# Kernel tuning notes

Hardware: AMD Instinct MI355X
Metric: run time of the kernel (lower is better)

Reference implementation:

```python
import jax, jax.numpy as jnp
import numpy as np

D_MODEL = 1024
RANK = 256
INIT_ALPHA = 0.5


def setup_inputs() -> dict:
    key = jax.random.key(0)
    ks = jax.random.split(key, 12)
    D, R = D_MODEL, RANK
    s = 0.02
    return {
        "x": jax.random.normal(ks[0], (4, 2048, D), dtype=jnp.float32),
        "Wq": jax.random.normal(ks[1], (D, D), dtype=jnp.float32) * s,
        "Wk": jax.random.normal(ks[2], (D, D), dtype=jnp.float32) * s,
        "Wo": jax.random.normal(ks[3], (D, D), dtype=jnp.float32) * s,
        "U_b": jax.random.normal(ks[4], (D, R), dtype=jnp.float32) * s,
        "V_b": jax.random.normal(ks[5], (D, R), dtype=jnp.float32) * s,
        "W_b": jax.random.normal(ks[6], (D, R), dtype=jnp.float32) * s,
        "bias_b": jnp.zeros((D,), dtype=jnp.float32),
        "U_t": jax.random.normal(ks[7], (D, R), dtype=jnp.float32) * s,
        "V_t": jax.random.normal(ks[8], (D, R), dtype=jnp.float32) * s,
        "W_t": jax.random.normal(ks[9], (D, R), dtype=jnp.float32) * s,
        "X_t": jax.random.normal(ks[10], (D, R), dtype=jnp.float32) * s,
        "bias_t": jnp.zeros((D,), dtype=jnp.float32),
        "alpha": jnp.asarray(INIT_ALPHA, dtype=jnp.float32),
    }


def reference(x, Wq, Wk, Wo, U_b, V_b, W_b, bias_b, U_t, V_t, W_t, X_t, bias_t, alpha):
    # Math identical to the original O(T^2 D) materialization (attention_mask=None path),
    # reduced to causal cumulative sums: sum_{j<=i} (q_i * k_j) = q_i * cumsum_j(k_j).
    B, T, D = x.shape
    Q = x @ Wq.T                      # [B,T,D] (nn.Linear: x @ W^T)
    K = x @ Wk.T
    counts = jnp.arange(1, T + 1, dtype=x.dtype)[None, :, None]  # [1,T,1]
    Z = jnp.cumsum(x, axis=1) / counts  # causal cumulative mean [B,T,D]

    # Bilinear: sum_{j<=i} ((Q_i V_b) * (K_j W_b)) U_b^T + bias_b (per j)
    a_b = Q @ V_b                     # [B,T,R]
    c_b = jnp.cumsum(K @ W_b, axis=1) # [B,T,R] causal sum over j
    bil = (a_b * c_b) @ U_b.T         # [B,T,D]

    # Trilinear: sum_{j<=i} ((Q_i V_t) * (K_j W_t) * (Z_i X_t)) U_t^T + bias_t
    a_t = Q @ V_t
    c_t = jnp.cumsum(K @ W_t, axis=1)
    z_t = Z @ X_t
    tri = (a_t * z_t * c_t) @ U_t.T   # [B,T,D]

    # Per-i division by n_valid = i+1; the per-(i,j) biases average back to themselves.
    out = (bil + alpha * tri) / counts + (bias_b + alpha * bias_t)
    return out @ Wo.T                 # W_O (dropout=0 -> identity)
```

## Files before the change

kernel.cpp:

```cpp
#include <hip/hip_runtime.h>

#define NBATCH  4
#define TSEQ    2048
#define MROWS   8192
#define NCAT    1280
#define NE      512

#define OFF_WQT   0u
#define OFF_WKT   524288u
#define OFF_WOB   1048576u
#define OFF_VCT   1572864u
#define OFF_WCT   1835008u
#define OFF_UCT   2097152u
#define OFF_B2    2359296u
#define OFF_PB    2360320u
#define OFF_GB    3015680u
#define OFF_Y     3277824u
#define OFF_SCR   13763584u
#define OFF_XB    13861888u
#define OFF_EB    OFF_XB

typedef __attribute__((ext_vector_type(8))) short bf16x8;
typedef __attribute__((ext_vector_type(4))) float f32x4;

__device__ __forceinline__ unsigned short f2bf(float f) {
  union { float f; unsigned u; } v; v.f = f;
  return (unsigned short)((v.u + 0x7fff + ((v.u >> 16) & 1)) >> 16);
}

__device__ __forceinline__ void gload16(const void* g, void* l) {
  __builtin_amdgcn_global_load_lds(
      (const __attribute__((address_space(1))) unsigned*)g,
      (__attribute__((address_space(3))) unsigned*)l, 16, 0, 0);
}

template <int EPI, int OBF, int CS>
__device__ __forceinline__ void mfma_tile(
    const short* __restrict__ A, const short* __restrict__ B, void* __restrict__ Cv,
    int K, int ldA, int ldB, int ldC, int m0, int n0,
    const float* __restrict__ bias, float* __restrict__ scr, short* L) {
  short* As = L;
  short* Bs = L + 8192;
  const int tid = threadIdx.x;
  const int l = tid & 63;
  const int wv = tid >> 6;
  const int wm = (wv >> 1) * 64, wn = (wv & 1) * 64;
  const int srow = tid >> 3;
  const int schk = tid & 7;
  const int arow = wm + (l & 15), brow = wn + (l & 15);
  const int kq = l >> 4;

  f32x4 acc[4][4] = {};

  for (int k0 = 0; k0 < K; k0 += 64) {
#pragma unroll
    for (int p = 0; p < 4; ++p) {
      const int r = p * 32 + srow;
      const int sw = (schk ^ (r & 7)) * 8;
      gload16(A + (size_t)(m0 + r) * ldA + k0 + sw, As + r * 64 + schk * 8);
      gload16(B + (size_t)(n0 + r) * ldB + k0 + sw, Bs + r * 64 + schk * 8);
    }
    __syncthreads();
#pragma unroll
    for (int h = 0; h < 2; ++h) {
      bf16x8 af[4], bfr[4];
#pragma unroll
      for (int m = 0; m < 4; ++m) {
        const int r = arow + m * 16;
        af[m] = *(const bf16x8*)&As[r * 64 + (((h * 4 + kq) ^ (r & 7)) * 8)];
      }
#pragma unroll
      for (int n = 0; n < 4; ++n) {
        const int r = brow + n * 16;
        bfr[n] = *(const bf16x8*)&Bs[r * 64 + (((h * 4 + kq) ^ (r & 7)) * 8)];
      }
#pragma unroll
      for (int m = 0; m < 4; ++m)
#pragma unroll
        for (int n = 0; n < 4; ++n)
          acc[m][n] = __builtin_amdgcn_mfma_f32_16x16x32_bf16(af[m], bfr[n], acc[m][n], 0, 0, 0);
    }
    __syncthreads();
  }

  const int cc = wn + (l & 15);
  const int crb = wm + (l >> 4) * 4;
#pragma unroll
  for (int m = 0; m < 4; ++m) {
#pragma unroll
    for (int j = 0; j < 4; ++j) {
      const int gm = m0 + crb + m * 16 + j;
      float inv = 1.0f;
      if (EPI) inv = 1.0f / (float)((gm & (TSEQ - 1)) + 1);
#pragma unroll
      for (int n = 0; n < 4; ++n) {
        const int gn = n0 + cc + n * 16;
        float v = acc[m][n][j];
        if (EPI) v = v * inv + bias[gn];
        if (OBF) ((short*)Cv)[(size_t)gm * ldC + gn] = (short)f2bf(v);
        else     ((float*)Cv)[(size_t)gm * ldC + gn] = v;
      }
    }
  }
  if (CS && n0 >= 512) {
    const int bb = (m0 + wm) >> 11;
    const int seg = ((m0 + wm) & (TSEQ - 1)) >> 6;
    float* sp = scr + (size_t)(bb * 32 + seg) * 768 + (n0 - 512);
#pragma unroll
    for (int n = 0; n < 4; ++n) {
      float s = 0.f;
#pragma unroll
      for (int m = 0; m < 4; ++m)
#pragma unroll
        for (int j = 0; j < 4; ++j) s += acc[m][n][j];
      s += __shfl_xor(s, 16, 64);
      s += __shfl_xor(s, 32, 64);
      if (l < 16) sp[cc + n * 16] = s;
    }
  }
}

template <int EPI, int CS>
__global__ __launch_bounds__(256) void mfma_nt(
    const short* __restrict__ A, const short* __restrict__ B,
    float* __restrict__ C, int K, int ldA, int ldB, int ldC,
    const float* __restrict__ bias, float* __restrict__ scr) {
  __shared__ short L[16384];
  mfma_tile<EPI, 0, CS>(A, B, C, K, ldA, ldB, ldC,
                        blockIdx.y * 128, blockIdx.x * 128, bias, scr, L);
}

__global__ __launch_bounds__(256) void prep_mfma(
    const short* __restrict__ VCT, const short* __restrict__ WQT,
    const short* __restrict__ WCT, const short* __restrict__ WKT,
    const short* __restrict__ WOB, const short* __restrict__ UCT,
    short* __restrict__ Pb, short* __restrict__ Gb) {
  __shared__ short L[16384];
  const int g = blockIdx.x >> 5, t = blockIdx.x & 31;
  if (g == 0)
    mfma_tile<0, 1, 0>(VCT, WQT, Pb, 1024, 1024, 1024, 1024,
                       (t >> 3) * 128, (t & 7) * 128, nullptr, nullptr, L);
  else if (g == 1)
    mfma_tile<0, 1, 0>(WCT, WKT, Pb + (size_t)512 * 1024, 1024, 1024, 1024, 1024,
                       (t >> 3) * 128, (t & 7) * 128, nullptr, nullptr, L);
  else
    mfma_tile<0, 1, 0>(WOB, UCT, Gb, 1024, 1024, 1024, 512,
                       (t >> 2) * 128, (t & 3) * 128, nullptr, nullptr, L);
}

__global__ __launch_bounds__(256) void prep_all(
    const float* __restrict__ Vb, const float* __restrict__ Vt,
    const float* __restrict__ Wb, const float* __restrict__ Wt,
    const float* __restrict__ Ub, const float* __restrict__ Ut,
    const float* __restrict__ Xt, const float* __restrict__ Wq,
    const float* __restrict__ Wk, const float* __restrict__ Wo,
    const float* __restrict__ x,
    const float* __restrict__ bias_b, const float* __restrict__ bias_t,
    const float* __restrict__ alpha_p,
    short* __restrict__ VCT, short* __restrict__ WCT, short* __restrict__ UCT,
    short* __restrict__ PbXt, short* __restrict__ WQT, short* __restrict__ WKT,
    short* __restrict__ WOB, short* __restrict__ xb, float* __restrict__ b2) {
  const int bid = blockIdx.x;
  const int tid = threadIdx.x;
  if (bid >= 10176) {
    const float al = *alpha_p;
    const int d = bid - 10176;
    float s = 0.f;
    for (int e = tid; e < 1024; e += 256)
      s += Wo[(size_t)d * 1024 + e] * (bias_b[e] + al * bias_t[e]);
    __shared__ float red[256];
    red[tid] = s; __syncthreads();
    for (int off = 128; off > 0; off >>= 1) {
      if (tid < off) red[tid] += red[tid + off];
      __syncthreads();
    }
    if (tid == 0) b2[d] = red[0];
    return;
  }
  if (bid >= 960) {
    const size_t j = ((size_t)(bid - 960) * 256 + tid) * 4;
    const int isWo = j < 1048576u;
    const float* s = isWo ? &Wo[j] : &x[j - 1048576u];
    const float4 v = *(const float4*)s;
    ushort4 o;
    o.x = f2bf(v.x); o.y = f2bf(v.y); o.z = f2bf(v.z); o.w = f2bf(v.w);
    unsigned short* dst = (unsigned short*)(isWo ? WOB : xb);
    *(ushort4*)&dst[isWo ? j : j - 1048576u] = o;
    return;
  }
  const float* src; short* O; int r0, d0, c0, ldS;
  if (bid < 384) {
    const int z = bid >> 7, t = bid & 127;
    r0 = (t >> 4) * 64; d0 = (t & 15) * 64; ldS = 256;
    const float* S0 = z == 0 ? Vb : z == 1 ? Wb : Ub;
    const float* S1 = z == 0 ? Vt : z == 1 ? Wt : Ut;
    O = z == 0 ? VCT : z == 1 ? WCT : UCT;
    src = (r0 < 256) ? S0 : S1; c0 = r0 & 255;
  } else if (bid < 448) {
    const int t = bid - 384;
    r0 = (t >> 4) * 64; d0 = (t & 15) * 64; ldS = 256;
    src = Xt; c0 = r0; O = PbXt;
  } else {
    const int t = bid - 448;
    const int w = t >> 8, tt = t & 255;
    r0 = (tt >> 4) * 64; d0 = (tt & 15) * 64; ldS = 1024;
    src = w ? Wk : Wq; O = w ? WKT : WQT; c0 = r0;
  }
  __shared__ float Ts[64][65];
  const int lr = tid >> 4;
  const int lc = (tid & 15) * 4;
#pragma unroll
  for (int p = 0; p < 4; ++p) {
    const int row = lr + p * 16;
    const float4 v = *(const float4*)&src[(size_t)(d0 + row) * ldS + c0 + lc];
    Ts[row][lc + 0] = v.x; Ts[row][lc + 1] = v.y;
    Ts[row][lc + 2] = v.z; Ts[row][lc + 3] = v.w;
  }
  __syncthreads();
#pragma unroll
  for (int p = 0; p < 4; ++p) {
    const int ri = lr + p * 16;
    ushort4 o;
    o.x = f2bf(Ts[lc + 0][ri]); o.y = f2bf(Ts[lc + 1][ri]);
    o.z = f2bf(Ts[lc + 2][ri]); o.w = f2bf(Ts[lc + 3][ri]);
    *(ushort4*)&((unsigned short*)O)[(size_t)(r0 + ri) * 1024 + d0 + lc] = o;
  }
}

__global__ void cumsum_s2(float* __restrict__ scr) {
  const int lane = threadIdx.x;
  const int cg = blockIdx.x, b = blockIdx.z;
  const int c = cg * 64 + lane;
  float run = 0.f;
  for (int seg = 0; seg < 32; ++seg) {
    const size_t idx = (size_t)(b * 32 + seg) * 768 + c;
    const float v = scr[idx];
    scr[idx] = run;
    run += v;
  }
}

__global__ __launch_bounds__(64) void scan_combine(
    const float* __restrict__ Y, const float* __restrict__ scr,
    short* __restrict__ Eb, const float* __restrict__ alpha_p) {
  const float al = *alpha_p;
  const int lane = threadIdx.x;
  const int g = blockIdx.x, seg = blockIdx.y, b = blockIdx.z;
  const int c2 = g * 64 + lane;
  const float* sc = scr + (size_t)(b * 32 + seg) * 768;
  float run_cb = sc[c2];
  float run_ct = sc[256 + c2];
  float run_zt = sc[512 + c2];
  const size_t row0 = (size_t)(b * TSEQ + seg * 64);
  const float* yr = Y + row0 * NCAT;
  float ab = yr[c2], at = yr[256 + c2];
  float cb = yr[512 + c2], ct = yr[768 + c2], zt = yr[1024 + c2];
  for (int tt = 0; tt < 64; ++tt) {
    float nab = 0, nat = 0, ncb = 0, nct = 0, nzt = 0;
    if (tt < 63) {
      const float* yn = yr + NCAT;
      nab = yn[c2]; nat = yn[256 + c2];
      ncb = yn[512 + c2]; nct = yn[768 + c2]; nzt = yn[1024 + c2];
    }
    run_cb += cb; run_ct += ct; run_zt += zt;
    const float inv = 1.0f / (float)(seg * 64 + tt + 1);
    short* er = Eb + (row0 + tt) * 512;
    er[c2]       = (short)f2bf(ab * run_cb);
    er[256 + c2] = (short)f2bf(al * at * (run_zt * inv) * run_ct);
    ab = nab; at = nat; cb = ncb; ct = nct; zt = nzt;
    yr += NCAT;
  }
}

extern "C" void kernel_launch(void* const* d_in, const int* in_sizes, int n_in,
                              void* d_out, int out_size, void* d_ws, size_t ws_size,
                              hipStream_t stream) {
  const float* x      = (const float*)d_in[0];
  const float* Wq     = (const float*)d_in[1];
  const float* Wk     = (const float*)d_in[2];
  const float* Wo     = (const float*)d_in[3];
  const float* Ub     = (const float*)d_in[4];
  const float* Vb     = (const float*)d_in[5];
  const float* Wb     = (const float*)d_in[6];
  const float* bias_b = (const float*)d_in[7];
  const float* Ut     = (const float*)d_in[8];
  const float* Vt     = (const float*)d_in[9];
  const float* Wt     = (const float*)d_in[10];
  const float* Xt     = (const float*)d_in[11];
  const float* bias_t = (const float*)d_in[12];
  const float* alpha  = (const float*)d_in[13];
  float* out = (float*)d_out;
  float* ws  = (float*)d_ws;

  short* WQT = (short*)(ws + OFF_WQT);
  short* WKT = (short*)(ws + OFF_WKT);
  short* WOB = (short*)(ws + OFF_WOB);
  short* VCT = (short*)(ws + OFF_VCT);
  short* WCT = (short*)(ws + OFF_WCT);
  short* UCT = (short*)(ws + OFF_UCT);
  float* b2  = ws + OFF_B2;
  short* Pb  = (short*)(ws + OFF_PB);
  short* Gb  = (short*)(ws + OFF_GB);
  float* Y   = ws + OFF_Y;
  float* scr = ws + OFF_SCR;
  short* xb  = (short*)(ws + OFF_XB);
  short* Eb  = (short*)(ws + OFF_EB);

  prep_all<<<11200, 256, 0, stream>>>(Vb, Vt, Wb, Wt, Ub, Ut, Xt, Wq, Wk, Wo, x,
                                      bias_b, bias_t, alpha,
                                      VCT, WCT, UCT, Pb + (size_t)1024 * 1024,
                                      WQT, WKT, WOB, xb, b2);
  prep_mfma<<<96, 256, 0, stream>>>(VCT, WQT, WCT, WKT, WOB, UCT, Pb, Gb);
  mfma_nt<0, 1><<<dim3(NCAT / 128, MROWS / 128), 256, 0, stream>>>(
      xb, Pb, Y, 1024, 1024, 1024, NCAT, nullptr, scr);
  cumsum_s2<<<dim3(12, 1, NBATCH), 64, 0, stream>>>(scr);
  scan_combine<<<dim3(4, 32, NBATCH), 64, 0, stream>>>(Y, scr, Eb, alpha);
  mfma_nt<1, 0><<<dim3(1024 / 128, MROWS / 128), 256, 0, stream>>>(
      Eb, Gb, out, 512, 512, 512, 1024, b2, nullptr);
}
```

Baseline: 221.0 us.

## Double-buffer MFMA GEMM tiles, add XCD block swizzle, widen scan_combine blocks

Replaces the single-buffered K-loop with a 32-wide, two-stage LDS double buffer. Async global-to-LDS loads for the next tile are issued before computing the current one, with explicit vmcnt waits and barriers, so memory latency can overlap MFMA work. Adds an XCD-aware remapping of block indices in the GEMM kernels to improve L2 locality across chiplets. Reshapes scan_combine to 256-thread blocks covering all 256 columns per segment. The hand-written waitcnt and barrier sequence depends on the exact count of outstanding loads, and the smaller K step means more barriers per tile.

```diff
diff --git a/kernel.cpp b/kernel.cpp
--- a/kernel.cpp
+++ b/kernel.cpp
@@ -39,49 +39,65 @@
     const short* __restrict__ A, const short* __restrict__ B, void* __restrict__ Cv,
     int K, int ldA, int ldB, int ldC, int m0, int n0,
     const float* __restrict__ bias, float* __restrict__ scr, short* L) {
-  short* As = L;
-  short* Bs = L + 8192;
   const int tid = threadIdx.x;
   const int l = tid & 63;
   const int wv = tid >> 6;
   const int wm = (wv >> 1) * 64, wn = (wv & 1) * 64;
-  const int srow = tid >> 3;
-  const int schk = tid & 7;
+  const int sr = tid >> 2;
+  const int sc4 = tid & 3;
   const int arow = wm + (l & 15), brow = wn + (l & 15);
   const int kq = l >> 4;
 
   f32x4 acc[4][4] = {};
 
-  for (int k0 = 0; k0 < K; k0 += 64) {
-#pragma unroll
-    for (int p = 0; p < 4; ++p) {
-      const int r = p * 32 + srow;
-      const int sw = (schk ^ (r & 7)) * 8;
-      gload16(A + (size_t)(m0 + r) * ldA + k0 + sw, As + r * 64 + schk * 8);
-      gload16(B + (size_t)(n0 + r) * ldB + k0 + sw, Bs + r * 64 + schk * 8);
-    }
-    __syncthreads();
-#pragma unroll
-    for (int h = 0; h < 2; ++h) {
-      bf16x8 af[4], bfr[4];
-#pragma unroll
-      for (int m = 0; m < 4; ++m) {
-        const int r = arow + m * 16;
-        af[m] = *(const bf16x8*)&As[r * 64 + (((h * 4 + kq) ^ (r & 7)) * 8)];
-      }
-#pragma unroll
-      for (int n = 0; n < 4; ++n) {
-        const int r = brow + n * 16;
-        bfr[n] = *(const bf16x8*)&Bs[r * 64 + (((h * 4 + kq) ^ (r & 7)) * 8)];
-      }
-#pragma unroll
-      for (int m = 0; m < 4; ++m)
-#pragma unroll
-        for (int n = 0; n < 4; ++n)
-          acc[m][n] = __builtin_amdgcn_mfma_f32_16x16x32_bf16(af[m], bfr[n], acc[m][n], 0, 0, 0);
-    }
-    __syncthreads();
-  }
+#define STAGE(k0, par) do {                                                  \
+    short* As_ = L + (par) * 8192;                                           \
+    short* Bs_ = As_ + 4096;                                                 \
+    _Pragma("unroll")                                                        \
+    for (int p = 0; p < 2; ++p) {                                            \
+      const int r = p * 64 + sr;                                             \
+      const int sw = (sc4 ^ (r & 3)) * 8;                                    \
+      gload16(A + (size_t)(m0 + r) * ldA + (k0) + sw, As_ + r * 32 + sc4 * 8); \
+      gload16(B + (size_t)(n0 + r) * ldB + (k0) + sw, Bs_ + r * 32 + sc4 * 8); \
+    }                                                                        \
+  } while (0)
+
+#define COMPUTE(par) do {                                                    \
+    short* As_ = L + (par) * 8192;                                           \
+    short* Bs_ = As_ + 4096;                                                 \
+    bf16x8 af[4], bfr[4];                                                    \
+    _Pragma("unroll")                                                        \
+    for (int m = 0; m < 4; ++m) {                                            \
+      const int r = arow + m * 16;                                           \
+      af[m] = *(const bf16x8*)&As_[r * 32 + ((kq ^ (r & 3)) * 8)];           \
+    }                                                                        \
+    _Pragma("unroll")                                                        \
+    for (int n = 0; n < 4; ++n) {                                            \
+      const int r = brow + n * 16;                                           \
+      bfr[n] = *(const bf16x8*)&Bs_[r * 32 + ((kq ^ (r & 3)) * 8)];          \
+    }                                                                        \
+    _Pragma("unroll")                                                        \
+    for (int m = 0; m < 4; ++m)                                              \
+      _Pragma("unroll")                                                      \
+      for (int n = 0; n < 4; ++n)                                            \
+        acc[m][n] = __builtin_amdgcn_mfma_f32_16x16x32_bf16(af[m], bfr[n], acc[m][n], 0, 0, 0); \
+  } while (0)
+
+  STAGE(0, 0);
+  const int nt = K >> 5;
+  for (int t = 0; t < nt; ++t) {
+    if (t + 1 < nt) {
+      STAGE((t + 1) << 5, (t + 1) & 1);
+      asm volatile("s_waitcnt vmcnt(4)" ::: "memory");
+    } else {
+      asm volatile("s_waitcnt vmcnt(0)" ::: "memory");
+    }
+    asm volatile("s_barrier" ::: "memory");
+    COMPUTE(t & 1);
+    asm volatile("s_barrier" ::: "memory");
+  }
+#undef STAGE
+#undef COMPUTE
 
   const int cc = wn + (l & 15);
   const int crb = wm + (l >> 4) * 4;
@@ -120,14 +136,25 @@
   }
 }
 
+__device__ __forceinline__ void xcd_swizzle(int& bx, int& by) {
+  const int gx = gridDim.x;
+  const int nwg = gx * gridDim.y;
+  const int n = by * gx + bx;
+  const int q = nwg >> 3;
+  const int s = (n & 7) * q + (n >> 3);
+  bx = s % gx; by = s / gx;
+}
+
 template <int EPI, int CS>
 __global__ __launch_bounds__(256) void mfma_nt(
     const short* __restrict__ A, const short* __restrict__ B,
     float* __restrict__ C, int K, int ldA, int ldB, int ldC,
     const float* __restrict__ bias, float* __restrict__ scr) {
   __shared__ short L[16384];
+  int bx = blockIdx.x, by = blockIdx.y;
+  xcd_swizzle(bx, by);
   mfma_tile<EPI, 0, CS>(A, B, C, K, ldA, ldB, ldC,
-                        blockIdx.y * 128, blockIdx.x * 128, bias, scr, L);
+                        by * 128, bx * 128, bias, scr, L);
 }
 
 __global__ __launch_bounds__(256) void prep_mfma(
@@ -240,13 +267,12 @@
   }
 }
 
-__global__ __launch_bounds__(64) void scan_combine(
+__global__ __launch_bounds__(256) void scan_combine(
     const float* __restrict__ Y, const float* __restrict__ scr,
     short* __restrict__ Eb, const float* __restrict__ alpha_p) {
   const float al = *alpha_p;
-  const int lane = threadIdx.x;
-  const int g = blockIdx.x, seg = blockIdx.y, b = blockIdx.z;
-  const int c2 = g * 64 + lane;
+  const int c2 = threadIdx.x;
+  const int seg = blockIdx.x, b = blockIdx.y;
   const float* sc = scr + (size_t)(b * 32 + seg) * 768;
   float run_cb = sc[c2];
   float run_ct = sc[256 + c2];
@@ -314,7 +340,7 @@
   mfma_nt<0, 1><<<dim3(NCAT / 128, MROWS / 128), 256, 0, stream>>>(
       xb, Pb, Y, 1024, 1024, 1024, NCAT, nullptr, scr);
   cumsum_s2<<<dim3(12, 1, NBATCH), 64, 0, stream>>>(scr);
-  scan_combine<<<dim3(4, 32, NBATCH), 64, 0, stream>>>(Y, scr, Eb, alpha);
+  scan_combine<<<dim3(32, NBATCH), 256, 0, stream>>>(Y, scr, Eb, alpha);
   mfma_nt<1, 0><<<dim3(1024 / 128, MROWS / 128), 256, 0, stream>>>(
       Eb, Gb, out, 512, 512, 512, 1024, b2, nullptr);
 }
```

Result: faster. 203.3 us (-8.0%).
